# Kernel optimization log

Measured on AMD Instinct MI355X. Metric: run time of the kernel, lower is better.

The kernel has to match this reference:

```python
import jax, jax.numpy as jnp
import numpy as np

NEG_BIG = -9e15

def setup_inputs() -> dict:
    key = jax.random.key(0)
    k1, k2, k3, k4 = jax.random.split(key, 4)
    N, F_in, F_out = 8192, 512, 128
    return {
        "input": jax.random.normal(k1, (N, F_in), dtype=jnp.float32),
        "adj": jax.random.randint(k2, (N, N), 0, 2, dtype=jnp.int32),
        "W": jax.random.normal(k3, (F_in, F_out), dtype=jnp.float32) * 0.05,
        "a": jax.random.normal(k4, (2 * F_out, 1), dtype=jnp.float32) * 0.05,
    }

def reference(input, adj, W, a):
    alpha = 0.2  # LeakyReLU negative slope
    h = input @ W                      # [N, F_out]
    F_out = h.shape[1]
    # concat score decomposition: a^T [h_i || h_j] = h_i @ a1 + h_j @ a2
    a1 = a[:F_out, 0]                  # [F_out]
    a2 = a[F_out:, 0]                  # [F_out]
    e = jax.nn.leaky_relu(h @ a1[:, None] + (h @ a2)[None, :], negative_slope=alpha)  # [N, N]
    e = jnp.where(adj > 0, e, NEG_BIG)
    attention = jax.nn.softmax(e, axis=1)
    h_prime = attention @ h            # [N, F_out]
    return jax.nn.elu(h_prime)         # concat=True
```

## Files before the change

kernel.cpp:

```cpp
#include <hip/hip_runtime.h>
#include <hip/hip_bf16.h>


typedef __attribute__((ext_vector_type(4))) float f32x4;
typedef __attribute__((ext_vector_type(8))) short s16x8;

#define N_NODES 8192
#define F_IN 512
#define F_OUT 128

static __device__ __forceinline__ short f2bf(float f) {
  __hip_bfloat16 h = __float2bfloat16(f);
  return __builtin_bit_cast(short, h);
}

__global__ void k0a_wt(const float* __restrict__ W, unsigned short* __restrict__ WT) {
  int idx = blockIdx.x * 256 + threadIdx.x;
  int k = idx >> 7, f = idx & 127;
  WT[(size_t)f * F_IN + k] = (unsigned short)f2bf(W[idx]);
}

__global__ void k0c_wa(const float* __restrict__ W, const float* __restrict__ a,
                       float* __restrict__ wa) {
  int k = blockIdx.x * 256 + threadIdx.x;
  if (k >= F_IN) return;
  const float* Wr = W + (size_t)k * F_OUT;
  float d1 = 0.f, d2 = 0.f;
#pragma unroll 8
  for (int f = 0; f < F_OUT; f += 4) {
    f32x4 w  = *(const f32x4*)(Wr + f);
    f32x4 a1 = *(const f32x4*)(a + f);
    f32x4 a2 = *(const f32x4*)(a + F_OUT + f);
    d1 += w[0] * a1[0] + w[1] * a1[1] + w[2] * a1[2] + w[3] * a1[3];
    d2 += w[0] * a2[0] + w[1] * a2[1] + w[2] * a2[2] + w[3] * a2[3];
  }
  wa[k] = d1;
  wa[F_IN + k] = d2;
}

__global__ __launch_bounds__(256) void k0b_x(const float* __restrict__ X,
    const float* __restrict__ wa, unsigned short* __restrict__ Xb,
    f32x4* __restrict__ rowdat, unsigned* __restrict__ pE) {
  int wave = threadIdx.x >> 6, lane = threadIdx.x & 63;
  int i = blockIdx.x * 4 + wave;
  const float* Xr = X + (size_t)i * F_IN + lane * 8;
  f32x4 x0 = ((const f32x4*)Xr)[0];
  f32x4 x1 = ((const f32x4*)Xr)[1];
  f32x4 w10 = ((const f32x4*)(wa + lane * 8))[0];
  f32x4 w11 = ((const f32x4*)(wa + lane * 8))[1];
  f32x4 w20 = ((const f32x4*)(wa + F_IN + lane * 8))[0];
  f32x4 w21 = ((const f32x4*)(wa + F_IN + lane * 8))[1];

  s16x8 xb;
#pragma unroll
  for (int e = 0; e < 4; e++) { xb[e] = f2bf(x0[e]); xb[e + 4] = f2bf(x1[e]); }
  *(s16x8*)(Xb + (size_t)i * F_IN + lane * 8) = xb;

  float d1 = 0.f, d2 = 0.f;
#pragma unroll
  for (int e = 0; e < 4; e++) {
    d1 += x0[e] * w10[e] + x1[e] * w11[e];
    d2 += x0[e] * w20[e] + x1[e] * w21[e];
  }
#pragma unroll
  for (int m = 1; m < 64; m <<= 1) {
    d1 += __shfl_xor(d1, m, 64);
    d2 += __shfl_xor(d2, m, 64);
  }
  if (lane == 0) {
    float s1 = d1, s2 = d2;
    f32x4 rd;
    rd[0] = expf(s1);
    rd[1] = expf(0.2f * s1);
    rd[2] = expf(-s1);
    rd[3] = 0.f;
    rowdat[i] = rd;
    unsigned e2  = (unsigned)(unsigned short)f2bf(expf(s2));
    unsigned e2s = (unsigned)(unsigned short)f2bf(expf(0.2f * s2));
    pE[i] = (e2s << 16) | e2;
  }
}

__global__ __launch_bounds__(256) void k1_gemm(const unsigned short* __restrict__ WT,
    const unsigned short* __restrict__ Xb, unsigned short* __restrict__ hT) {
  int wave = threadIdx.x >> 6, lane = threadIdx.x & 63;
  int lrow = lane & 15, grp = lane >> 4;
  int g = blockIdx.x >> 1;
  int ftile = (blockIdx.x & 1) * 4 + wave;

  const unsigned short* Ar = WT + (size_t)(ftile * 16 + lrow) * F_IN + grp * 8;
  const unsigned short* Br = Xb + (size_t)(g * 64 + lrow) * F_IN + grp * 8;

  f32x4 acc[4];
#pragma unroll
  for (int nt = 0; nt < 4; nt++) acc[nt] = (f32x4)(0.0f);

  for (int k0 = 0; k0 < F_IN; k0 += 32) {
    s16x8 af = *(const s16x8*)(Ar + k0);
#pragma unroll
    for (int nt = 0; nt < 4; nt++) {
      s16x8 bf = *(const s16x8*)(Br + (size_t)nt * 16 * F_IN + k0);
      acc[nt] = __builtin_amdgcn_mfma_f32_16x16x32_bf16(af, bf, acc[nt], 0, 0, 0);
    }
  }
#pragma unroll
  for (int nt = 0; nt < 4; nt++)
#pragma unroll
    for (int r = 0; r < 4; r++)
      hT[(size_t)(ftile * 16 + grp * 4 + r) * N_NODES + g * 64 + nt * 16 + lrow] =
          (unsigned short)f2bf(acc[nt][r]);
}

template <int JS>
__global__ __launch_bounds__(256) void k2_main(const int* __restrict__ adj,
    const unsigned short* __restrict__ hT, const f32x4* __restrict__ rowdat,
    const unsigned* __restrict__ pE, float* __restrict__ accws,
    float* __restrict__ denws) {
  constexpr int JCHUNK = N_NODES / JS;
  int js = blockIdx.x & (JS - 1);
  int rb = blockIdx.x / JS;
  int wave = threadIdx.x >> 6, lane = threadIdx.x & 63;
  int lrow = lane & 15, grp = lane >> 4;
  int waveRow = rb * 64 + wave * 16;
  int i0 = waveRow + lrow;

  f32x4 rd = rowdat[i0];
  float E1 = rd[0], E1s = rd[1], T1 = rd[2];
  const int* adjRow = adj + (size_t)i0 * N_NODES;
  int jlo = js * JCHUNK;

  f32x4 acc[8];
#pragma unroll
  for (int n = 0; n < 8; n++) acc[n] = (f32x4)(0.0f);
  float dsum = 0.f;

#define PROC(adjv, pe, e)                                            \
  {                                                                  \
    unsigned pu = (pe);                                              \
    float E2  = __builtin_bit_cast(float, pu << 16);                 \
    float E2s = __builtin_bit_cast(float, pu & 0xffff0000u);         \
    float p = (E2 > T1) ? E1 * E2 : E1s * E2s;                       \
    p = ((adjv) != 0) ? p : 0.f;                                     \
    dsum += p;                                                       \
    af[e] = f2bf(p);                                                 \
  }

  for (int j0 = jlo; j0 < jlo + JCHUNK; j0 += 32) {
    int jj = j0 + grp * 8;
    const int4* ap = (const int4*)(adjRow + jj);
    int4 A0 = ap[0];
    int4 A1 = ap[1];
    const uint4* pp = (const uint4*)(pE + jj);
    uint4 P0 = pp[0];
    uint4 P1 = pp[1];
    s16x8 af;
    PROC(A0.x, P0.x, 0); PROC(A0.y, P0.y, 1);
    PROC(A0.z, P0.z, 2); PROC(A0.w, P0.w, 3);
    PROC(A1.x, P1.x, 4); PROC(A1.y, P1.y, 5);
    PROC(A1.z, P1.z, 6); PROC(A1.w, P1.w, 7);
    const unsigned short* hTj = hT + jj;
#pragma unroll
    for (int n = 0; n < 8; n++) {
      s16x8 bf = *(const s16x8*)(hTj + (size_t)(n * 16 + lrow) * N_NODES);
      acc[n] = __builtin_amdgcn_mfma_f32_16x16x32_bf16(af, bf, acc[n], 0, 0, 0);
    }
  }
#undef PROC

  dsum += __shfl_xor(dsum, 16, 64);
  dsum += __shfl_xor(dsum, 32, 64);
  if (lane < 16) denws[js * N_NODES + waveRow + lane] = dsum;

#pragma unroll
  for (int n = 0; n < 8; n++)
#pragma unroll
    for (int r = 0; r < 4; r++)
      accws[((size_t)js * N_NODES + waveRow + grp * 4 + r) * F_OUT + n * 16 + lrow] =
          acc[n][r];
}

template <int JS>
__global__ void k3_fin(const float* __restrict__ accws,
                       const float* __restrict__ denws, float* __restrict__ out) {
  int idx = blockIdx.x * 256 + threadIdx.x;
  int i = idx >> 7;
  const int S = N_NODES * F_OUT;
  float s = 0.f, d = 0.f;
#pragma unroll
  for (int js = 0; js < JS; js++) {
    s += accws[idx + (size_t)js * S];
    d += denws[i + js * N_NODES];
  }
  float v = s / d;
  out[idx] = v > 0.f ? v : expm1f(v);
}

extern "C" void kernel_launch(void* const* d_in, const int* in_sizes, int n_in,
                              void* d_out, int out_size, void* d_ws, size_t ws_size,
                              hipStream_t stream) {
  const float* X   = (const float*)d_in[0];
  const int*   adj = (const int*)d_in[1];
  const float* W   = (const float*)d_in[2];
  const float* a   = (const float*)d_in[3];
  float* out = (float*)d_out;

  char* ws = (char*)d_ws;
  size_t off = 0;
  unsigned short* WT = (unsigned short*)(ws + off); off += (size_t)F_OUT * F_IN * 2;
  unsigned short* Xb = (unsigned short*)(ws + off); off += (size_t)N_NODES * F_IN * 2;
  unsigned short* hT = (unsigned short*)(ws + off); off += (size_t)F_OUT * N_NODES * 2;
  f32x4* rowdat = (f32x4*)(ws + off); off += (size_t)N_NODES * 16;
  unsigned* pE = (unsigned*)(ws + off); off += (size_t)N_NODES * 4;
  float* wa = (float*)(ws + off); off += (size_t)2 * F_IN * 4;
  float* accws = (float*)(ws + off);
  size_t base = off;
  (void)in_sizes; (void)n_in; (void)out_size;

  k0a_wt<<<(F_IN * F_OUT) / 256, 256, 0, stream>>>(W, WT);
  k0c_wa<<<2, 256, 0, stream>>>(W, a, wa);
  k0b_x<<<N_NODES / 4, 256, 0, stream>>>(X, wa, Xb, rowdat, pE);
  k1_gemm<<<(N_NODES / 64) * 2, 256, 0, stream>>>(WT, Xb, hT);

  size_t need16 = base + 16ull * ((size_t)N_NODES * F_OUT * 4 + N_NODES * 4);
  if (ws_size >= need16) {
    constexpr int JS = 16;
    float* denws = (float*)(ws + base + (size_t)JS * N_NODES * F_OUT * 4);
    k2_main<JS><<<(N_NODES / 64) * JS, 256, 0, stream>>>(adj, hT, rowdat, pE, accws, denws);
    k3_fin<JS><<<(N_NODES * F_OUT) / 256, 256, 0, stream>>>(accws, denws, out);
  } else {
    constexpr int JS = 4;
    float* denws = (float*)(ws + base + (size_t)JS * N_NODES * F_OUT * 4);
    k2_main<JS><<<(N_NODES / 64) * JS, 256, 0, stream>>>(adj, hT, rowdat, pE, accws, denws);
    k3_fin<JS><<<(N_NODES * F_OUT) / 256, 256, 0, stream>>>(accws, denws, out);
  }
}
```

Baseline: 542.8 us.

## Precompute adjacency bitmask and stream it in attention kernel with fewer j-splits

```diff
diff --git a/kernel.cpp b/kernel.cpp
--- a/kernel.cpp
+++ b/kernel.cpp
@@ -8,10 +8,27 @@
 #define N_NODES 8192
 #define F_IN 512
 #define F_OUT 128
+#define JS 8
+#define JCHUNK (N_NODES / JS)
 
 static __device__ __forceinline__ short f2bf(float f) {
   __hip_bfloat16 h = __float2bfloat16(f);
   return __builtin_bit_cast(short, h);
+}
+
+__global__ __launch_bounds__(256) void k_mask(const int* __restrict__ adj,
+    unsigned long long* __restrict__ mask) {
+  const int nwaves = gridDim.x * 4;
+  int wid = blockIdx.x * 4 + (threadIdx.x >> 6);
+  int lane = threadIdx.x & 63;
+  const int ntasks = N_NODES * (N_NODES / 64);
+  for (int task = wid; task < ntasks; task += nwaves) {
+    int row = task >> 7;
+    int cg = task & 127;
+    int v = adj[(size_t)row * N_NODES + cg * 64 + lane];
+    unsigned long long b = __ballot(v != 0);
+    if (lane == 0) mask[(size_t)row * (N_NODES / 64) + cg] = b;
+  }
 }
 
 __global__ void k0a_wt(const float* __restrict__ W, unsigned short* __restrict__ WT) {
@@ -85,84 +102,80 @@
     const unsigned short* __restrict__ Xb, unsigned short* __restrict__ hT) {
   int wave = threadIdx.x >> 6, lane = threadIdx.x & 63;
   int lrow = lane & 15, grp = lane >> 4;
-  int g = blockIdx.x >> 1;
-  int ftile = (blockIdx.x & 1) * 4 + wave;
-
-  const unsigned short* Ar = WT + (size_t)(ftile * 16 + lrow) * F_IN + grp * 8;
-  const unsigned short* Br = Xb + (size_t)(g * 64 + lrow) * F_IN + grp * 8;
-
-  f32x4 acc[4];
-#pragma unroll
-  for (int nt = 0; nt < 4; nt++) acc[nt] = (f32x4)(0.0f);
-
+  int tile = blockIdx.x * 4 + wave;
+  int fb = tile & 7;
+  int nb = tile >> 3;
+
+  const unsigned short* Ar = WT + (size_t)(fb * 16 + lrow) * F_IN + grp * 8;
+  const unsigned short* Br = Xb + (size_t)(nb * 16 + lrow) * F_IN + grp * 8;
+
+  f32x4 acc = (f32x4)(0.0f);
+#pragma unroll
   for (int k0 = 0; k0 < F_IN; k0 += 32) {
     s16x8 af = *(const s16x8*)(Ar + k0);
-#pragma unroll
-    for (int nt = 0; nt < 4; nt++) {
-      s16x8 bf = *(const s16x8*)(Br + (size_t)nt * 16 * F_IN + k0);
-      acc[nt] = __builtin_amdgcn_mfma_f32_16x16x32_bf16(af, bf, acc[nt], 0, 0, 0);
-    }
-  }
-#pragma unroll
-  for (int nt = 0; nt < 4; nt++)
-#pragma unroll
-    for (int r = 0; r < 4; r++)
-      hT[(size_t)(ftile * 16 + grp * 4 + r) * N_NODES + g * 64 + nt * 16 + lrow] =
-          (unsigned short)f2bf(acc[nt][r]);
-}
-
-template <int JS>
-__global__ __launch_bounds__(256) void k2_main(const int* __restrict__ adj,
+    s16x8 bf = *(const s16x8*)(Br + k0);
+    acc = __builtin_amdgcn_mfma_f32_16x16x32_bf16(af, bf, acc, 0, 0, 0);
+  }
+#pragma unroll
+  for (int r = 0; r < 4; r++)
+    hT[(size_t)(fb * 16 + grp * 4 + r) * N_NODES + nb * 16 + lrow] =
+        (unsigned short)f2bf(acc[r]);
+}
+
+__global__ __launch_bounds__(256, 4) void k2_main(const unsigned* __restrict__ mask32,
     const unsigned short* __restrict__ hT, const f32x4* __restrict__ rowdat,
     const unsigned* __restrict__ pE, float* __restrict__ accws,
     float* __restrict__ denws) {
-  constexpr int JCHUNK = N_NODES / JS;
   int js = blockIdx.x & (JS - 1);
   int rb = blockIdx.x / JS;
   int wave = threadIdx.x >> 6, lane = threadIdx.x & 63;
   int lrow = lane & 15, grp = lane >> 4;
   int waveRow = rb * 64 + wave * 16;
   int i0 = waveRow + lrow;
+  int jlo = js * JCHUNK;
 
   f32x4 rd = rowdat[i0];
   float E1 = rd[0], E1s = rd[1], T1 = rd[2];
-  const int* adjRow = adj + (size_t)i0 * N_NODES;
-  int jlo = js * JCHUNK;
 
   f32x4 acc[8];
 #pragma unroll
   for (int n = 0; n < 8; n++) acc[n] = (f32x4)(0.0f);
   float dsum = 0.f;
 
-#define PROC(adjv, pe, e)                                            \
+#define PROC(pe, e)                                                  \
   {                                                                  \
     unsigned pu = (pe);                                              \
     float E2  = __builtin_bit_cast(float, pu << 16);                 \
     float E2s = __builtin_bit_cast(float, pu & 0xffff0000u);         \
-    float p = (E2 > T1) ? E1 * E2 : E1s * E2s;                       \
-    p = ((adjv) != 0) ? p : 0.f;                                     \
+    float sel = (E2 > T1) ? E1 * E2 : E1s * E2s;                     \
+    float p = ((b >> e) & 1u) ? sel : 0.f;                           \
     dsum += p;                                                       \
     af[e] = f2bf(p);                                                 \
   }
 
-  for (int j0 = jlo; j0 < jlo + JCHUNK; j0 += 32) {
-    int jj = j0 + grp * 8;
-    const int4* ap = (const int4*)(adjRow + jj);
-    int4 A0 = ap[0];
-    int4 A1 = ap[1];
-    const uint4* pp = (const uint4*)(pE + jj);
-    uint4 P0 = pp[0];
-    uint4 P1 = pp[1];
-    s16x8 af;
-    PROC(A0.x, P0.x, 0); PROC(A0.y, P0.y, 1);
-    PROC(A0.z, P0.z, 2); PROC(A0.w, P0.w, 3);
-    PROC(A1.x, P1.x, 4); PROC(A1.y, P1.y, 5);
-    PROC(A1.z, P1.z, 6); PROC(A1.w, P1.w, 7);
-    const unsigned short* hTj = hT + jj;
-#pragma unroll
-    for (int n = 0; n < 8; n++) {
-      s16x8 bf = *(const s16x8*)(hTj + (size_t)(n * 16 + lrow) * N_NODES);
-      acc[n] = __builtin_amdgcn_mfma_f32_16x16x32_bf16(af, bf, acc[n], 0, 0, 0);
+  for (int sc = 0; sc < JCHUNK / 512; sc++) {
+    int jbase = jlo + sc * 512;
+    const uint4* mrow =
+        (const uint4*)(mask32 + (size_t)i0 * (N_NODES / 32) + jbase / 32);
+    uint4 mm[4];
+#pragma unroll
+    for (int c = 0; c < 4; c++) mm[c] = mrow[c];
+
+#pragma unroll
+    for (int t = 0; t < 16; t++) {
+      int jj = jbase + t * 32 + grp * 8;
+      unsigned b = (mm[t >> 2][t & 3] >> (grp * 8)) & 0xffu;
+      const uint4* pp = (const uint4*)(pE + jj);
+      uint4 P0 = pp[0], P1 = pp[1];
+      s16x8 af;
+      PROC(P0.x, 0); PROC(P0.y, 1); PROC(P0.z, 2); PROC(P0.w, 3);
+      PROC(P1.x, 4); PROC(P1.y, 5); PROC(P1.z, 6); PROC(P1.w, 7);
+      const unsigned short* hTj = hT + jj;
+#pragma unroll
+      for (int n = 0; n < 8; n++) {
+        s16x8 bf = *(const s16x8*)(hTj + (size_t)(n * 16 + lrow) * N_NODES);
+        acc[n] = __builtin_amdgcn_mfma_f32_16x16x32_bf16(af, bf, acc[n], 0, 0, 0);
+      }
     }
   }
 #undef PROC
@@ -179,20 +192,22 @@
           acc[n][r];
 }
 
-template <int JS>
 __global__ void k3_fin(const float* __restrict__ accws,
                        const float* __restrict__ denws, float* __restrict__ out) {
-  int idx = blockIdx.x * 256 + threadIdx.x;
-  int i = idx >> 7;
-  const int S = N_NODES * F_OUT;
-  float s = 0.f, d = 0.f;
+  int idx4 = blockIdx.x * 256 + threadIdx.x;
+  int i = idx4 >> 5;
+  const int S4 = N_NODES * F_OUT / 4;
+  f32x4 s = (f32x4)(0.0f);
+  float d = 0.f;
 #pragma unroll
   for (int js = 0; js < JS; js++) {
-    s += accws[idx + (size_t)js * S];
+    s += ((const f32x4*)accws)[idx4 + js * S4];
     d += denws[i + js * N_NODES];
   }
-  float v = s / d;
-  out[idx] = v > 0.f ? v : expm1f(v);
+  f32x4 v = s / d;
+#pragma unroll
+  for (int e = 0; e < 4; e++) v[e] = v[e] > 0.f ? v[e] : expm1f(v[e]);
+  ((f32x4*)out)[idx4] = v;
 }
 
 extern "C" void kernel_launch(void* const* d_in, const int* in_sizes, int n_in,
@@ -212,25 +227,18 @@
   f32x4* rowdat = (f32x4*)(ws + off); off += (size_t)N_NODES * 16;
   unsigned* pE = (unsigned*)(ws + off); off += (size_t)N_NODES * 4;
   float* wa = (float*)(ws + off); off += (size_t)2 * F_IN * 4;
-  float* accws = (float*)(ws + off);
-  size_t base = off;
-  (void)in_sizes; (void)n_in; (void)out_size;
-
+  unsigned long long* mask = (unsigned long long*)(ws + off);
+  off += (size_t)N_NODES * (N_NODES / 64) * 8;
+  float* accws = (float*)(ws + off); off += (size_t)JS * N_NODES * F_OUT * 4;
+  float* denws = (float*)(ws + off); off += (size_t)JS * N_NODES * 4;
+  (void)in_sizes; (void)n_in; (void)out_size; (void)ws_size;
+
+  k_mask<<<2048, 256, 0, stream>>>(adj, mask);
   k0a_wt<<<(F_IN * F_OUT) / 256, 256, 0, stream>>>(W, WT);
   k0c_wa<<<2, 256, 0, stream>>>(W, a, wa);
   k0b_x<<<N_NODES / 4, 256, 0, stream>>>(X, wa, Xb, rowdat, pE);
-  k1_gemm<<<(N_NODES / 64) * 2, 256, 0, stream>>>(WT, Xb, hT);
-
-  size_t need16 = base + 16ull * ((size_t)N_NODES * F_OUT * 4 + N_NODES * 4);
-  if (ws_size >= need16) {
-    constexpr int JS = 16;
-    float* denws = (float*)(ws + base + (size_t)JS * N_NODES * F_OUT * 4);
-    k2_main<JS><<<(N_NODES / 64) * JS, 256, 0, stream>>>(adj, hT, rowdat, pE, accws, denws);
-    k3_fin<JS><<<(N_NODES * F_OUT) / 256, 256, 0, stream>>>(accws, denws, out);
-  } else {
-    constexpr int JS = 4;
-    float* denws = (float*)(ws + base + (size_t)JS * N_NODES * F_OUT * 4);
-    k2_main<JS><<<(N_NODES / 64) * JS, 256, 0, stream>>>(adj, hT, rowdat, pE, accws, denws);
-    k3_fin<JS><<<(N_NODES * F_OUT) / 256, 256, 0, stream>>>(accws, denws, out);
-  }
-}
+  k1_gemm<<<1024, 256, 0, stream>>>(WT, Xb, hT);
+  k2_main<<<(N_NODES / 64) * JS, 256, 0, stream>>>((const unsigned*)mask, hT,
+                                                   rowdat, pE, accws, denws);
+  k3_fin<<<(N_NODES * F_OUT) / 4 / 256, 256, 0, stream>>>(accws, denws, out);
+}
```

Result: no change. 552.1 us (+1.7%).
